# Kernel optimization log

Measured on AMD Instinct MI355X. Metric: run time of the kernel, lower is better.

Reference implementation:

```python
import jax, jax.numpy as jnp
import numpy as np
from jax import lax

B, C, H, W = 32, 256, 96, 96
G = 2            # num_groups
K = 3            # kernel_size
R = 4            # reduction_ratio
CR = C // R
BN_EPS = 1e-5


def setup_inputs() -> dict:
    key = jax.random.key(0)
    ks = jax.random.split(key, 10)
    inp = {
        "x": jax.random.normal(ks[0], (B, C, H, W), dtype=jnp.float32),
        # dynamic depthwise weight bank and bias bank
        "dyn_weight": jax.random.normal(ks[1], (G, C, K, K), dtype=jnp.float32) * 0.02,
        "dyn_bias": jax.random.normal(ks[2], (G, C), dtype=jnp.float32) * 0.02,
        # proj: ConvModule(C -> C//R, 1x1, BN, GELU)  [conv has no bias since BN follows]
        "w1": jax.random.normal(ks[3], (CR, C), dtype=jnp.float32) * (1.0 / np.sqrt(C)),
        "bn_gamma": jnp.ones((CR,), dtype=jnp.float32),
        "bn_beta": jnp.zeros((CR,), dtype=jnp.float32),
        "bn_mean": jax.random.normal(ks[4], (CR,), dtype=jnp.float32) * 0.1,
        "bn_var": jax.random.uniform(ks[5], (CR,), dtype=jnp.float32, minval=0.5, maxval=1.5),
        # second 1x1 conv: C//R -> C*G, with bias
        "w2": jax.random.normal(ks[6], (C * G, CR), dtype=jnp.float32) * (1.0 / np.sqrt(CR)),
        "b2": jnp.zeros((C * G,), dtype=jnp.float32),
    }
    return inp


def _proj(p, w1, bn_gamma, bn_beta, bn_mean, bn_var, w2, b2):
    # p: [B, C, h, w] -> [B, C*G, h, w]; 1x1 conv -> BN(eval) -> GELU -> 1x1 conv
    h = jnp.einsum('bchw,oc->bohw', p, w1)
    inv = bn_gamma * lax.rsqrt(bn_var + BN_EPS)
    h = h * inv[None, :, None, None] + (bn_beta - bn_mean * inv)[None, :, None, None]
    h = jax.nn.gelu(h, approximate=False)
    return jnp.einsum('bohw,no->bnhw', h, w2) + b2[None, :, None, None]


def reference(x, dyn_weight, dyn_bias, w1, bn_gamma, bn_beta, bn_mean, bn_var, w2, b2):
    # AdaptiveAvgPool2d to (K, K); H, W divisible by K -> uniform block average
    pooled = x.reshape(B, C, K, H // K, K, W // K).mean(axis=(3, 5))  # [B,C,K,K]

    # per-sample depthwise weights via softmax mixture over G weight banks
    scale = _proj(pooled, w1, bn_gamma, bn_beta, bn_mean, bn_var, w2, b2)
    scale = jax.nn.softmax(scale.reshape(B, G, C, K, K), axis=1)
    weight = jnp.sum(scale * dyn_weight[None], axis=1)  # [B,C,K,K]

    # per-sample bias via global-average-pooled features
    gap = x.mean(axis=(2, 3), keepdims=True)  # [B,C,1,1]
    bscale = _proj(gap, w1, bn_gamma, bn_beta, bn_mean, bn_var, w2, b2)
    bscale = jax.nn.softmax(bscale.reshape(B, G, C), axis=1)
    bias = jnp.sum(bscale * dyn_bias[None], axis=1)  # [B,C]

    # grouped conv with groups = B*C (per-sample depthwise)
    xr = x.reshape(1, B * C, H, W)
    wr = weight.reshape(B * C, 1, K, K)
    y = lax.conv_general_dilated(
        xr, wr, window_strides=(1, 1),
        padding=[(K // 2, K // 2), (K // 2, K // 2)],
        feature_group_count=B * C,
        dimension_numbers=('NCHW', 'OIHW', 'NCHW'))
    return y.reshape(B, C, H, W) + bias[:, :, None, None]
```

## Files before the change

### kernel.cpp

```cpp
#include <hip/hip_runtime.h>
#include <math.h>

#define B_ 32
#define C_ 256
#define HW_ 96
#define G_ 2
#define K_ 3
#define CR_ 64
#define IMG_ (HW_*HW_)
#define BN_EPS 1e-5f

__global__ __launch_bounds__(256) void pool_kernel(const float* __restrict__ x,
                                                   float* __restrict__ pooled) {
    int wg = blockIdx.x;
    int bh = wg % 3;
    int bc = wg / 3;
    const float4* src = (const float4*)(x + (size_t)bc * IMG_ + (size_t)bh * 32 * HW_);
    int t = threadIdx.x;
    float a0 = 0.f, a1 = 0.f, a2 = 0.f;
    #pragma unroll
    for (int k = 0; k < 3; ++k) {
        int f = t + 256 * k;
        float4 v = src[f];
        float s = v.x + v.y + v.z + v.w;
        int colq = f % 24;
        int bin = colq >> 3;
        a0 += (bin == 0) ? s : 0.f;
        a1 += (bin == 1) ? s : 0.f;
        a2 += (bin == 2) ? s : 0.f;
    }
    #pragma unroll
    for (int off = 32; off > 0; off >>= 1) {
        a0 += __shfl_down(a0, off);
        a1 += __shfl_down(a1, off);
        a2 += __shfl_down(a2, off);
    }
    __shared__ float red[3][4];
    int wave = t >> 6, lane = t & 63;
    if (lane == 0) { red[0][wave] = a0; red[1][wave] = a1; red[2][wave] = a2; }
    __syncthreads();
    if (t < 3) {
        float s = red[t][0] + red[t][1] + red[t][2] + red[t][3];
        pooled[(size_t)bc * 9 + bh * 3 + t] = s * (1.0f / 1024.0f);
    }
}

__global__ __launch_bounds__(256) void proj_kernel(
    const float* __restrict__ pooled,
    const float* __restrict__ dyn_w,
    const float* __restrict__ dyn_b,
    const float* __restrict__ w1,
    const float* __restrict__ bn_g, const float* __restrict__ bn_b,
    const float* __restrict__ bn_m, const float* __restrict__ bn_v,
    const float* __restrict__ w2,
    const float* __restrict__ b2,
    float* __restrict__ wout,
    float* __restrict__ bout)
{
    int b = blockIdx.x;
    __shared__ float pool[C_][10];
    __shared__ float hbuf[CR_][10];
    int t = threadIdx.x;

    {
        const float* p = pooled + ((size_t)b * C_ + t) * 9;
        float s = 0.f;
        #pragma unroll
        for (int i = 0; i < 9; ++i) { float v = p[i]; pool[t][i] = v; s += v; }
        pool[t][9] = s * (1.0f / 9.0f);
    }
    __syncthreads();

    for (int task = t; task < CR_ * 10; task += 256) {
        int o = task & 63, pos = task >> 6;
        const float4* wr = (const float4*)(w1 + (size_t)o * C_);
        float acc = 0.f;
        #pragma unroll 8
        for (int i = 0; i < C_ / 4; ++i) {
            float4 wv = wr[i];
            acc += wv.x * pool[4*i][pos] + wv.y * pool[4*i+1][pos]
                 + wv.z * pool[4*i+2][pos] + wv.w * pool[4*i+3][pos];
        }
        float inv = bn_g[o] * rsqrtf(bn_v[o] + BN_EPS);
        float hv = acc * inv + (bn_b[o] - bn_m[o] * inv);
        hv = 0.5f * hv * (1.0f + erff(hv * 0.70710678118654752f));
        hbuf[o][pos] = hv;
    }
    __syncthreads();

    for (int task = t; task < C_ * 10; task += 256) {
        int c = task & 255, pos = task >> 8;
        const float4* r0 = (const float4*)(w2 + (size_t)c * CR_);
        const float4* r1 = (const float4*)(w2 + (size_t)(C_ + c) * CR_);
        float s0 = b2[c], s1 = b2[C_ + c];
        #pragma unroll 8
        for (int i = 0; i < CR_ / 4; ++i) {
            float4 v0 = r0[i], v1 = r1[i];
            float h0 = hbuf[4*i][pos], h1 = hbuf[4*i+1][pos];
            float h2 = hbuf[4*i+2][pos], h3 = hbuf[4*i+3][pos];
            s0 += v0.x*h0 + v0.y*h1 + v0.z*h2 + v0.w*h3;
            s1 += v1.x*h0 + v1.y*h1 + v1.z*h2 + v1.w*h3;
        }
        float m = fmaxf(s0, s1);
        float e0 = expf(s0 - m), e1 = expf(s1 - m);
        float p0 = e0 / (e0 + e1), p1 = 1.0f - p0;
        if (pos < 9) {
            wout[((size_t)b * C_ + c) * 9 + pos] =
                p0 * dyn_w[(size_t)c * 9 + pos] + p1 * dyn_w[(size_t)(C_ * 9) + c * 9 + pos];
        } else {
            bout[(size_t)b * C_ + c] = p0 * dyn_b[c] + p1 * dyn_b[C_ + c];
        }
    }
}

#define TW 98
__global__ __launch_bounds__(256) void dwconv_kernel(const float* __restrict__ x,
                                                     const float* __restrict__ wgt,
                                                     const float* __restrict__ bias,
                                                     float* __restrict__ out) {
    int bc = blockIdx.x;
    __shared__ float tile[TW * TW];
    int t = threadIdx.x;

    for (int i = t; i < TW * TW; i += 256) tile[i] = 0.f;
    __syncthreads();

    const float4* src = (const float4*)(x + (size_t)bc * IMG_);
    #pragma unroll
    for (int k = 0; k < 9; ++k) {
        int f = t + 256 * k;
        float4 v = src[f];
        int r = f / 24, cq = f % 24;
        float* d = &tile[(r + 1) * TW + 1 + 4 * cq];
        d[0] = v.x; d[1] = v.y; d[2] = v.z; d[3] = v.w;
    }

    float w[9];
    #pragma unroll
    for (int i = 0; i < 9; ++i) w[i] = wgt[(size_t)bc * 9 + i];
    float bs = bias[bc];
    __syncthreads();

    float4* dst = (float4*)(out + (size_t)bc * IMG_);
    #pragma unroll
    for (int k = 0; k < 9; ++k) {
        int f = t + 256 * k;
        int r = f / 24, cq = f % 24;
        const float* base = &tile[r * TW + 4 * cq];
        float a0 = bs, a1 = bs, a2 = bs, a3 = bs;
        #pragma unroll
        for (int dh = 0; dh < 3; ++dh) {
            const float* row = base + dh * TW;
            float i0 = row[0], i1 = row[1], i2 = row[2];
            float i3 = row[3], i4 = row[4], i5 = row[5];
            float w0 = w[dh*3], w1v = w[dh*3+1], w2v = w[dh*3+2];
            a0 += i0*w0 + i1*w1v + i2*w2v;
            a1 += i1*w0 + i2*w1v + i3*w2v;
            a2 += i2*w0 + i3*w1v + i4*w2v;
            a3 += i3*w0 + i4*w1v + i5*w2v;
        }
        dst[f] = make_float4(a0, a1, a2, a3);
    }
}

extern "C" void kernel_launch(void* const* d_in, const int* in_sizes, int n_in,
                              void* d_out, int out_size, void* d_ws, size_t ws_size,
                              hipStream_t stream) {
    const float* x     = (const float*)d_in[0];
    const float* dyn_w = (const float*)d_in[1];
    const float* dyn_b = (const float*)d_in[2];
    const float* w1    = (const float*)d_in[3];
    const float* bn_g  = (const float*)d_in[4];
    const float* bn_b  = (const float*)d_in[5];
    const float* bn_m  = (const float*)d_in[6];
    const float* bn_v  = (const float*)d_in[7];
    const float* w2    = (const float*)d_in[8];
    const float* b2    = (const float*)d_in[9];
    float* out = (float*)d_out;

    float* ws = (float*)d_ws;
    float* pooled = ws;
    float* weight = ws + (size_t)B_ * C_ * 9;
    float* bias   = weight + (size_t)B_ * C_ * 9;

    pool_kernel<<<B_ * C_ * 3, 256, 0, stream>>>(x, pooled);
    proj_kernel<<<B_, 256, 0, stream>>>(pooled, dyn_w, dyn_b, w1, bn_g, bn_b,
                                        bn_m, bn_v, w2, b2, weight, bias);
    dwconv_kernel<<<B_ * C_, 256, 0, stream>>>(x, weight, bias, out);
}
```

Before: 620.1 us.

## Replace LDS-tiled depthwise conv with register sliding-window over rows

```diff
diff --git a/kernel.cpp b/kernel.cpp
--- a/kernel.cpp
+++ b/kernel.cpp
@@ -113,54 +113,61 @@
     }
 }
 
-#define TW 98
-__global__ __launch_bounds__(256) void dwconv_kernel(const float* __restrict__ x,
+__global__ __launch_bounds__(192) void dwconv_kernel(const float* __restrict__ x,
                                                      const float* __restrict__ wgt,
                                                      const float* __restrict__ bias,
                                                      float* __restrict__ out) {
     int bc = blockIdx.x;
-    __shared__ float tile[TW * TW];
     int t = threadIdx.x;
+    int qc = t % 24;
+    int rg = t / 24;
+    int r0 = rg * 12;
 
-    for (int i = t; i < TW * TW; i += 256) tile[i] = 0.f;
-    __syncthreads();
-
-    const float4* src = (const float4*)(x + (size_t)bc * IMG_);
-    #pragma unroll
-    for (int k = 0; k < 9; ++k) {
-        int f = t + 256 * k;
-        float4 v = src[f];
-        int r = f / 24, cq = f % 24;
-        float* d = &tile[(r + 1) * TW + 1 + 4 * cq];
-        d[0] = v.x; d[1] = v.y; d[2] = v.z; d[3] = v.w;
-    }
+    const float* img = x + (size_t)bc * IMG_;
+    float4* dst = (float4*)(out + (size_t)bc * IMG_);
 
     float w[9];
     #pragma unroll
     for (int i = 0; i < 9; ++i) w[i] = wgt[(size_t)bc * 9 + i];
     float bs = bias[bc];
-    __syncthreads();
 
-    float4* dst = (float4*)(out + (size_t)bc * IMG_);
+    float A[6], Bv[6], Cv[6];
+
+    #define LOADROW(r, d)                                                    \
+        do {                                                                 \
+            int _r = (r);                                                    \
+            if ((unsigned)_r < (unsigned)HW_) {                              \
+                const float* _p = img + _r * HW_ + 4 * qc;                   \
+                float4 _v = *(const float4*)_p;                              \
+                d[1] = _v.x; d[2] = _v.y; d[3] = _v.z; d[4] = _v.w;          \
+                d[0] = (qc > 0)  ? _p[-1] : 0.f;                             \
+                d[5] = (qc < 23) ? _p[4]  : 0.f;                             \
+            } else {                                                         \
+                d[0] = d[1] = d[2] = d[3] = d[4] = d[5] = 0.f;               \
+            }                                                                \
+        } while (0)
+
+    LOADROW(r0 - 1, A);
+    LOADROW(r0,     Bv);
+
     #pragma unroll
-    for (int k = 0; k < 9; ++k) {
-        int f = t + 256 * k;
-        int r = f / 24, cq = f % 24;
-        const float* base = &tile[r * TW + 4 * cq];
-        float a0 = bs, a1 = bs, a2 = bs, a3 = bs;
+    for (int i = 0; i < 12; ++i) {
+        int r = r0 + i;
+        LOADROW(r + 1, Cv);
+        float4 o;
+        o.x = bs; o.y = bs; o.z = bs; o.w = bs;
         #pragma unroll
-        for (int dh = 0; dh < 3; ++dh) {
-            const float* row = base + dh * TW;
-            float i0 = row[0], i1 = row[1], i2 = row[2];
-            float i3 = row[3], i4 = row[4], i5 = row[5];
-            float w0 = w[dh*3], w1v = w[dh*3+1], w2v = w[dh*3+2];
-            a0 += i0*w0 + i1*w1v + i2*w2v;
-            a1 += i1*w0 + i2*w1v + i3*w2v;
-            a2 += i2*w0 + i3*w1v + i4*w2v;
-            a3 += i3*w0 + i4*w1v + i5*w2v;
+        for (int j = 0; j < 3; ++j) {
+            o.x += A[j]  * w[j] + Bv[j]  * w[3+j] + Cv[j]  * w[6+j];
+            o.y += A[j+1]* w[j] + Bv[j+1]* w[3+j] + Cv[j+1]* w[6+j];
+            o.z += A[j+2]* w[j] + Bv[j+2]* w[3+j] + Cv[j+2]* w[6+j];
+            o.w += A[j+3]* w[j] + Bv[j+3]* w[3+j] + Cv[j+3]* w[6+j];
         }
-        dst[f] = make_float4(a0, a1, a2, a3);
+        dst[r * 24 + qc] = o;
+        #pragma unroll
+        for (int j = 0; j < 6; ++j) { A[j] = Bv[j]; Bv[j] = Cv[j]; }
     }
+    #undef LOADROW
 }
 
 extern "C" void kernel_launch(void* const* d_in, const int* in_sizes, int n_in,
@@ -186,5 +193,5 @@
     pool_kernel<<<B_ * C_ * 3, 256, 0, stream>>>(x, pooled);
     proj_kernel<<<B_, 256, 0, stream>>>(pooled, dyn_w, dyn_b, w1, bn_g, bn_b,
                                         bn_m, bn_v, w2, b2, weight, bias);
-    dwconv_kernel<<<B_ * C_, 256, 0, stream>>>(x, weight, bias, out);
+    dwconv_kernel<<<B_ * C_, 192, 0, stream>>>(x, weight, bias, out);
 }
```

Result: no change. 618.9 us (-0.2%).
